# Kernel optimization log

Measured on AMD Instinct MI355X. Metric: run time of the kernel, lower is better.

Reference implementation:

```python
import jax, jax.numpy as jnp
import numpy as np

BS, ZDIM, HID, TLEN = 1024, 256, 256, 128


def setup_inputs() -> dict:
    key = jax.random.key(0)
    k1, k2, k3 = jax.random.split(key, 3)
    z0 = jax.random.normal(k1, (BS, ZDIM), dtype=jnp.float32)
    # strictly increasing time grid on [0, 1]
    t = jnp.linspace(0.0, 1.0, TLEN).astype(jnp.float32)
    # small init keeps the 127-step RK4 trajectory numerically stable
    W1 = jax.random.normal(k2, (ZDIM, HID), dtype=jnp.float32) * (0.5 / np.sqrt(ZDIM))
    b1 = jnp.zeros((HID,), dtype=jnp.float32)
    W2 = jax.random.normal(k3, (HID, ZDIM), dtype=jnp.float32) * (0.5 / np.sqrt(HID))
    b2 = jnp.zeros((ZDIM,), dtype=jnp.float32)
    return {"z0": z0, "t": t, "W1": W1, "b1": b1, "W2": W2, "b2": b2}


def reference(z0, t, W1, b1, W2, b2):
    # ODEF: f(z, t) = tanh(z @ W1 + b1) @ W2 + b2  (autonomous MLP dynamics)
    def f(z, ti):
        return jnp.tanh(z @ W1 + b1) @ W2 + b2

    def rk4_step(z, ts):
        t0, t1 = ts
        h = t1 - t0
        k1 = f(z, t0)
        k2 = f(z + k1 * (h * 0.5), t0 + h * 0.5)
        k3 = f(z + k2 * (h * 0.5), t0 + h * 0.5)
        k4 = f(z + k3 * h, t0 + h)
        zn = z + (h / 6.0) * (k1 + 2.0 * k2 + 2.0 * k3 + k4)
        return zn, None
    # sequential integration over time_len-1 intervals (matches the python loop)
    zT, _ = jax.lax.scan(rk4_step, z0, (t[:-1], t[1:]))
    # NeuralODE.forward default: return_whole_sequence=False -> z[-1]
    return zT
```

## Files before the change

kernel.cpp:

```cpp
#include <hip/hip_runtime.h>
#include <hip/hip_bf16.h>


#define BS   1024
#define ZDIM 256
#define TLEN 128
#define ROWSTRIDE 264

typedef short v8s __attribute__((ext_vector_type(8)));
typedef float v4f __attribute__((ext_vector_type(4)));

static __device__ __forceinline__ ushort f2bf_rne(float x) {
    union { float f; unsigned u; } v; v.f = x;
    unsigned r = v.u + 0x7FFFu + ((v.u >> 16) & 1u);
    return (ushort)(r >> 16);
}

static __device__ __forceinline__ unsigned pk2(float a, float b) {
    union { __hip_bfloat162 h; unsigned u; } cv;
    cv.h = __float22bfloat162_rn(make_float2(a, b));
    return cv.u;
}

static __device__ __forceinline__ float fast_tanh(float x) {
    float e = __builtin_amdgcn_exp2f(2.88539008177793f * x);
    float r = __builtin_amdgcn_rcpf(e + 1.0f);
    return 1.0f - 2.0f * r;
}

__global__ __launch_bounds__(512, 1)
void ode_mfma_kernel(const float* __restrict__ z0,
                     const float* __restrict__ t,
                     const float* __restrict__ W1,
                     const float* __restrict__ b1,
                     const float* __restrict__ W2,
                     const float* __restrict__ b2,
                     float* __restrict__ out)
{
    __shared__ ushort zbuf[16 * ROWSTRIDE];
    __shared__ ushort hbuf[16 * ROWSTRIDE];

    const int tid  = threadIdx.x;
    const int wv   = tid >> 6;
    const int lane = tid & 63;
    const int q    = lane >> 4;
    const int ln   = lane & 15;
    const int rowbase = blockIdx.x * 16;

    v8s w1f[2][8], w2f[2][8];
    #pragma unroll
    for (int ct = 0; ct < 2; ++ct) {
        const int c = wv * 32 + ct * 16 + ln;
        #pragma unroll
        for (int ks = 0; ks < 8; ++ks) {
            v8s a, b;
            #pragma unroll
            for (int j = 0; j < 8; ++j) {
                const int k = ks * 32 + q * 8 + j;
                a[j] = (short)f2bf_rne(W1[k * ZDIM + c]);
                b[j] = (short)f2bf_rne(W2[k * ZDIM + c]);
            }
            w1f[ct][ks] = a;
            w2f[ct][ks] = b;
        }
    }

    v4f b1f[2], b2f[2];
    #pragma unroll
    for (int ct = 0; ct < 2; ++ct)
        #pragma unroll
        for (int r = 0; r < 4; ++r) {
            b1f[ct][r] = b1[wv * 32 + ct * 16 + q * 4 + r];
            b2f[ct][r] = b2[wv * 32 + ct * 16 + q * 4 + r];
        }

    const int rdbase = ln * ROWSTRIDE + q * 8;
    const int wrbase = ln * ROWSTRIDE + wv * 32 + q * 4;

    float zloc[2][4];
    #pragma unroll
    for (int ct = 0; ct < 2; ++ct) {
        #pragma unroll
        for (int r = 0; r < 4; ++r)
            zloc[ct][r] = z0[(rowbase + ln) * ZDIM + wv * 32 + ct * 16 + q * 4 + r];
        uint2 p; p.x = pk2(zloc[ct][0], zloc[ct][1]); p.y = pk2(zloc[ct][2], zloc[ct][3]);
        *(uint2*)&zbuf[wrbase + ct * 16] = p;
    }
    __syncthreads();

    float kacc[2][4];

    #pragma unroll 1
    for (int step = 0; step < TLEN - 1; ++step) {
        const float h = t[step + 1] - t[step];

        #pragma unroll
        for (int stage = 0; stage < 4; ++stage) {
            v4f acc0 = b1f[0], acc1 = b1f[1];
            #pragma unroll
            for (int ks = 0; ks < 8; ++ks) {
                const v8s zf = *(const v8s*)&zbuf[rdbase + ks * 32];
                acc0 = __builtin_amdgcn_mfma_f32_16x16x32_bf16(w1f[0][ks], zf, acc0, 0, 0, 0);
                acc1 = __builtin_amdgcn_mfma_f32_16x16x32_bf16(w1f[1][ks], zf, acc1, 0, 0, 0);
            }
            {
                uint2 p0, p1;
                p0.x = pk2(fast_tanh(acc0[0]), fast_tanh(acc0[1]));
                p0.y = pk2(fast_tanh(acc0[2]), fast_tanh(acc0[3]));
                p1.x = pk2(fast_tanh(acc1[0]), fast_tanh(acc1[1]));
                p1.y = pk2(fast_tanh(acc1[2]), fast_tanh(acc1[3]));
                *(uint2*)&hbuf[wrbase]      = p0;
                *(uint2*)&hbuf[wrbase + 16] = p1;
            }
            __syncthreads();

            v4f f0 = b2f[0], f1 = b2f[1];
            #pragma unroll
            for (int ks = 0; ks < 8; ++ks) {
                const v8s hf = *(const v8s*)&hbuf[rdbase + ks * 32];
                f0 = __builtin_amdgcn_mfma_f32_16x16x32_bf16(w2f[0][ks], hf, f0, 0, 0, 0);
                f1 = __builtin_amdgcn_mfma_f32_16x16x32_bf16(w2f[1][ks], hf, f1, 0, 0, 0);
            }

            #pragma unroll
            for (int ct = 0; ct < 2; ++ct) {
                float zn[4];
                #pragma unroll
                for (int r = 0; r < 4; ++r) {
                    const float f = (ct == 0) ? f0[r] : f1[r];
                    if (stage == 0) {
                        kacc[ct][r] = f;
                        zn[r] = zloc[ct][r] + 0.5f * h * f;
                    } else if (stage == 1) {
                        kacc[ct][r] += 2.0f * f;
                        zn[r] = zloc[ct][r] + 0.5f * h * f;
                    } else if (stage == 2) {
                        kacc[ct][r] += 2.0f * f;
                        zn[r] = zloc[ct][r] + h * f;
                    } else {
                        kacc[ct][r] += f;
                        zloc[ct][r] += (h * (1.0f / 6.0f)) * kacc[ct][r];
                        zn[r] = zloc[ct][r];
                    }
                }
                uint2 p; p.x = pk2(zn[0], zn[1]); p.y = pk2(zn[2], zn[3]);
                *(uint2*)&zbuf[wrbase + ct * 16] = p;
            }
            __syncthreads();
        }
    }

    #pragma unroll
    for (int ct = 0; ct < 2; ++ct)
        #pragma unroll
        for (int r = 0; r < 4; ++r)
            out[(rowbase + ln) * ZDIM + wv * 32 + ct * 16 + q * 4 + r] = zloc[ct][r];
}

extern "C" void kernel_launch(void* const* d_in, const int* in_sizes, int n_in,
                              void* d_out, int out_size, void* d_ws, size_t ws_size,
                              hipStream_t stream) {
    const float* z0 = (const float*)d_in[0];
    const float* t  = (const float*)d_in[1];
    const float* W1 = (const float*)d_in[2];
    const float* b1 = (const float*)d_in[3];
    const float* W2 = (const float*)d_in[4];
    const float* b2 = (const float*)d_in[5];
    float* out = (float*)d_out;

    dim3 grid(BS / 16);
    dim3 block(512);
    hipLaunchKernelGGL(ode_mfma_kernel, grid, block, 0, stream,
                       z0, t, W1, b1, W2, b2, out);
}
```

Measured before the change: 532.9 us.

## Halve block to 4 waves, each computing 64 columns with register-resident weights

Each block now runs 4 wavefronts instead of 8, and each wave holds four 16-column tiles of W1 and W2 in registers. This halves the number of waves taking part in each __syncthreads barrier and gives more independent MFMA chains per wave, so more instruction-level parallelism per LDS fragment read. Per-wave register pressure doubles: 64 v8s weight fragments is about 256 VGPRs for weights alone, which risks spills, and per-block MFMA throughput may fall because fewer SIMDs are active. The time grid is also copied into shared memory so h is not reloaded from global memory each step.

```diff
diff --git a/kernel.cpp b/kernel.cpp
--- a/kernel.cpp
+++ b/kernel.cpp
@@ -28,7 +28,7 @@
     return 1.0f - 2.0f * r;
 }
 
-__global__ __launch_bounds__(512, 1)
+__global__ __launch_bounds__(256, 1)
 void ode_mfma_kernel(const float* __restrict__ z0,
                      const float* __restrict__ t,
                      const float* __restrict__ W1,
@@ -39,6 +39,7 @@
 {
     __shared__ ushort zbuf[16 * ROWSTRIDE];
     __shared__ ushort hbuf[16 * ROWSTRIDE];
+    __shared__ float  tsh[TLEN];
 
     const int tid  = threadIdx.x;
     const int wv   = tid >> 6;
@@ -47,10 +48,12 @@
     const int ln   = lane & 15;
     const int rowbase = blockIdx.x * 16;
 
-    v8s w1f[2][8], w2f[2][8];
+    if (tid < TLEN) tsh[tid] = t[tid];
+
+    v8s w1f[4][8], w2f[4][8];
     #pragma unroll
-    for (int ct = 0; ct < 2; ++ct) {
-        const int c = wv * 32 + ct * 16 + ln;
+    for (int ct = 0; ct < 4; ++ct) {
+        const int c = wv * 64 + ct * 16 + ln;
         #pragma unroll
         for (int ks = 0; ks < 8; ++ks) {
             v8s a, b;
@@ -65,69 +68,75 @@
         }
     }
 
-    v4f b1f[2], b2f[2];
+    v4f b1f[4], b2f[4];
     #pragma unroll
-    for (int ct = 0; ct < 2; ++ct)
+    for (int ct = 0; ct < 4; ++ct)
         #pragma unroll
         for (int r = 0; r < 4; ++r) {
-            b1f[ct][r] = b1[wv * 32 + ct * 16 + q * 4 + r];
-            b2f[ct][r] = b2[wv * 32 + ct * 16 + q * 4 + r];
+            b1f[ct][r] = b1[wv * 64 + ct * 16 + q * 4 + r];
+            b2f[ct][r] = b2[wv * 64 + ct * 16 + q * 4 + r];
         }
 
     const int rdbase = ln * ROWSTRIDE + q * 8;
-    const int wrbase = ln * ROWSTRIDE + wv * 32 + q * 4;
+    const int wrbase = ln * ROWSTRIDE + wv * 64 + q * 4;
 
-    float zloc[2][4];
+    float zloc[4][4];
     #pragma unroll
-    for (int ct = 0; ct < 2; ++ct) {
+    for (int ct = 0; ct < 4; ++ct) {
         #pragma unroll
         for (int r = 0; r < 4; ++r)
-            zloc[ct][r] = z0[(rowbase + ln) * ZDIM + wv * 32 + ct * 16 + q * 4 + r];
+            zloc[ct][r] = z0[(rowbase + ln) * ZDIM + wv * 64 + ct * 16 + q * 4 + r];
         uint2 p; p.x = pk2(zloc[ct][0], zloc[ct][1]); p.y = pk2(zloc[ct][2], zloc[ct][3]);
         *(uint2*)&zbuf[wrbase + ct * 16] = p;
     }
     __syncthreads();
 
-    float kacc[2][4];
+    float kacc[4][4];
 
     #pragma unroll 1
     for (int step = 0; step < TLEN - 1; ++step) {
-        const float h = t[step + 1] - t[step];
+        const float h = tsh[step + 1] - tsh[step];
 
         #pragma unroll
         for (int stage = 0; stage < 4; ++stage) {
-            v4f acc0 = b1f[0], acc1 = b1f[1];
+            v4f acc[4];
+            #pragma unroll
+            for (int ct = 0; ct < 4; ++ct) acc[ct] = b1f[ct];
             #pragma unroll
             for (int ks = 0; ks < 8; ++ks) {
                 const v8s zf = *(const v8s*)&zbuf[rdbase + ks * 32];
-                acc0 = __builtin_amdgcn_mfma_f32_16x16x32_bf16(w1f[0][ks], zf, acc0, 0, 0, 0);
-                acc1 = __builtin_amdgcn_mfma_f32_16x16x32_bf16(w1f[1][ks], zf, acc1, 0, 0, 0);
+                #pragma unroll
+                for (int ct = 0; ct < 4; ++ct)
+                    acc[ct] = __builtin_amdgcn_mfma_f32_16x16x32_bf16(
+                        w1f[ct][ks], zf, acc[ct], 0, 0, 0);
             }
-            {
-                uint2 p0, p1;
-                p0.x = pk2(fast_tanh(acc0[0]), fast_tanh(acc0[1]));
-                p0.y = pk2(fast_tanh(acc0[2]), fast_tanh(acc0[3]));
-                p1.x = pk2(fast_tanh(acc1[0]), fast_tanh(acc1[1]));
-                p1.y = pk2(fast_tanh(acc1[2]), fast_tanh(acc1[3]));
-                *(uint2*)&hbuf[wrbase]      = p0;
-                *(uint2*)&hbuf[wrbase + 16] = p1;
+            #pragma unroll
+            for (int ct = 0; ct < 4; ++ct) {
+                uint2 p;
+                p.x = pk2(fast_tanh(acc[ct][0]), fast_tanh(acc[ct][1]));
+                p.y = pk2(fast_tanh(acc[ct][2]), fast_tanh(acc[ct][3]));
+                *(uint2*)&hbuf[wrbase + ct * 16] = p;
             }
             __syncthreads();
 
-            v4f f0 = b2f[0], f1 = b2f[1];
+            v4f fac[4];
+            #pragma unroll
+            for (int ct = 0; ct < 4; ++ct) fac[ct] = b2f[ct];
             #pragma unroll
             for (int ks = 0; ks < 8; ++ks) {
                 const v8s hf = *(const v8s*)&hbuf[rdbase + ks * 32];
-                f0 = __builtin_amdgcn_mfma_f32_16x16x32_bf16(w2f[0][ks], hf, f0, 0, 0, 0);
-                f1 = __builtin_amdgcn_mfma_f32_16x16x32_bf16(w2f[1][ks], hf, f1, 0, 0, 0);
+                #pragma unroll
+                for (int ct = 0; ct < 4; ++ct)
+                    fac[ct] = __builtin_amdgcn_mfma_f32_16x16x32_bf16(
+                        w2f[ct][ks], hf, fac[ct], 0, 0, 0);
             }
 
             #pragma unroll
-            for (int ct = 0; ct < 2; ++ct) {
+            for (int ct = 0; ct < 4; ++ct) {
                 float zn[4];
                 #pragma unroll
                 for (int r = 0; r < 4; ++r) {
-                    const float f = (ct == 0) ? f0[r] : f1[r];
+                    const float f = fac[ct][r];
                     if (stage == 0) {
                         kacc[ct][r] = f;
                         zn[r] = zloc[ct][r] + 0.5f * h * f;
@@ -151,10 +160,10 @@
     }
 
     #pragma unroll
-    for (int ct = 0; ct < 2; ++ct)
+    for (int ct = 0; ct < 4; ++ct)
         #pragma unroll
         for (int r = 0; r < 4; ++r)
-            out[(rowbase + ln) * ZDIM + wv * 32 + ct * 16 + q * 4 + r] = zloc[ct][r];
+            out[(rowbase + ln) * ZDIM + wv * 64 + ct * 16 + q * 4 + r] = zloc[ct][r];
 }
 
 extern "C" void kernel_launch(void* const* d_in, const int* in_sizes, int n_in,
@@ -169,7 +178,7 @@
     float* out = (float*)d_out;
 
     dim3 grid(BS / 16);
-    dim3 block(512);
+    dim3 block(256);
     hipLaunchKernelGGL(ode_mfma_kernel, grid, block, 0, stream,
                        z0, t, W1, b1, W2, b2, out);
 }
```

Result: slower. 710.1 us (+33.3%).
